# Optimization experiments

Hardware: AMD Instinct MI355X
Metric: run time of the kernel (lower is better)

Reference implementation:

```python
import jax, jax.numpy as jnp
import numpy as np

N = 100000      # num nodes
E = 1600000     # num edges
NFEAT = 512
NHID = 256
NCLASS = 32
K = 10
ALPHA = 0.1


def setup_inputs() -> dict:
    key = jax.random.key(0)
    ks = jax.random.split(key, 6)
    x = jax.random.normal(ks[0], (N, NFEAT), dtype=jnp.float32)
    edge_index = jax.random.randint(ks[1], (2, E), 0, N, dtype=jnp.int32)
    edge_attr = jax.random.uniform(ks[2], (E,), dtype=jnp.float32)
    # Linear params (Kaiming-ish scale)
    W_start = jax.random.normal(ks[3], (NFEAT, NHID), dtype=jnp.float32) * np.float32(1.0 / np.sqrt(NFEAT))
    b_start = jnp.zeros((NHID,), jnp.float32)
    W_end = jax.random.normal(ks[4], (NHID, NCLASS), dtype=jnp.float32) * np.float32(1.0 / np.sqrt(NHID))
    b_end = jnp.zeros((NCLASS,), jnp.float32)
    # GPR 'PPR' init coefficients: temp[k] = alpha*(1-alpha)^k, temp[K] = (1-alpha)^K
    temp = (ALPHA * (1.0 - ALPHA) ** np.arange(K + 1)).astype(np.float32)
    temp[-1] = np.float32((1.0 - ALPHA) ** K)
    temp = jnp.asarray(temp)
    return {"x": x, "edge_attr": edge_attr, "W_start": W_start, "b_start": b_start,
            "W_end": W_end, "b_end": b_end, "temp": temp, "edge_index": edge_index}


def gcn_norm(edge_index, edge_weight, num_nodes):
    # add self loops with weight 1 (PyG default fill_value=1)
    loop = jnp.arange(num_nodes, dtype=edge_index.dtype)
    ei = jnp.concatenate([edge_index, jnp.stack([loop, loop])], axis=1)   # [2, E+N]
    ew = jnp.concatenate([edge_weight, jnp.ones((num_nodes,), edge_weight.dtype)])
    row, col = ei[0], ei[1]
    deg = jax.ops.segment_sum(ew, col, num_segments=num_nodes)            # [N]
    dis = jnp.where(deg > 0, jax.lax.rsqrt(jnp.where(deg > 0, deg, 1.0)), 0.0)
    norm = dis[row] * ew * dis[col]                                       # [E+N]
    return ei, norm


def reference(x, edge_attr, W_start, b_start, W_end, b_end, temp, edge_index):
    # MLP front-end (eval mode: dropout is identity)
    h = jax.nn.relu(x @ W_start + b_start)        # [N, NHID]
    h = jax.nn.relu(h @ W_end + b_end)            # [N, NCLASS]
    ei, norm = gcn_norm(edge_index, edge_attr, N)
    row, col = ei[0], ei[1]
    hidden = h * temp[0]
    xk = h
    for k in range(K):
        # SpMM: gather messages norm * x[row], scatter-add at col
        xk = jax.ops.segment_sum(norm[:, None] * xk[row], col, num_segments=N)
        hidden = hidden + temp[k + 1] * xk
    return hidden
```

## Files before the change

kernel.cpp:

```cpp
#include <hip/hip_runtime.h>

typedef __attribute__((ext_vector_type(8))) short short8;
typedef __attribute__((ext_vector_type(4))) float f32x4;
typedef unsigned long long u64;

constexpr int NN = 100000;
constexpr int EE = 1600000;
constexpr int NF = 512;
constexpr int NH = 256;
constexpr int NC = 32;
constexpr int KP = 10;
constexpr int PKN = EE + 8 * NN;
constexpr int GB = 782;

__device__ __forceinline__ unsigned short f2bf(float f) {
  unsigned int u = __float_as_uint(f);
  u += 0x7FFFu + ((u >> 16) & 1u);
  return (unsigned short)(u >> 16);
}
__device__ __forceinline__ float bf2f(unsigned short s) {
  return __uint_as_float(((unsigned int)s) << 16);
}
__device__ __forceinline__ int padc(int c) { return (c + 7) & ~7; }

__device__ __forceinline__ short8 cvt8(float4 a0, float4 a1) {
  union { unsigned int u[4]; short8 s; } r;
  asm("v_cvt_pk_bf16_f32 %0, %1, %2" : "=v"(r.u[0]) : "v"(a0.x), "v"(a0.y));
  asm("v_cvt_pk_bf16_f32 %0, %1, %2" : "=v"(r.u[1]) : "v"(a0.z), "v"(a0.w));
  asm("v_cvt_pk_bf16_f32 %0, %1, %2" : "=v"(r.u[2]) : "v"(a1.x), "v"(a1.y));
  asm("v_cvt_pk_bf16_f32 %0, %1, %2" : "=v"(r.u[3]) : "v"(a1.z), "v"(a1.w));
  return r.s;
}

__device__ __forceinline__ void block_sync_lds() {
  asm volatile("s_waitcnt lgkmcnt(0)" ::: "memory");
  __builtin_amdgcn_s_barrier();
}

__global__ void prep_kernel(const float* __restrict__ Ws, const float* __restrict__ We,
                            unsigned short* __restrict__ Wt, unsigned short* __restrict__ Web,
                            u64* __restrict__ dc, u64* __restrict__ pk) {
  if (blockIdx.x < 32) {
    __shared__ float tile[64][65];
    const int k0 = (blockIdx.x >> 2) * 64;
    const int c0 = (blockIdx.x & 3) * 64;
    const int t = threadIdx.x;
    const int g = t >> 6, l = t & 63;
#pragma unroll
    for (int j = 0; j < 16; j++) {
      const int row = g * 16 + j;
      tile[row][l] = Ws[(size_t)(k0 + row) * NH + c0 + l];
    }
    __syncthreads();
    const int col = t >> 2, ks = (t & 3) * 16;
    union { unsigned short us[16]; short8 s8[2]; } st;
#pragma unroll
    for (int i = 0; i < 16; i++) st.us[i] = f2bf(tile[ks + i][col]);
    unsigned short* dst = Wt + (size_t)(c0 + col) * NF + k0 + ks;
    *reinterpret_cast<short8*>(dst) = st.s8[0];
    *reinterpret_cast<short8*>(dst + 8) = st.s8[1];
  } else if (blockIdx.x == 32) {
    const int t = threadIdx.x;
    const int col = t & 31, kb = (t >> 5) * 32;
#pragma unroll
    for (int i = 0; i < 32; i++)
      Web[(size_t)col * 256 + kb + i] = f2bf(We[(size_t)(kb + i) * NC + col]);
  } else {
    const int i = (blockIdx.x - 33) * 256 + threadIdx.x;
    if (i < NN) dc[i] = (1ULL << 44) | (1ULL << 32);
    for (int j = i; j < PKN; j += 391 * 256) pk[j] = 0;
  }
}

__global__ __launch_bounds__(512, 2) void gemm_deg_kernel(
    const float* __restrict__ X, const unsigned short* __restrict__ Wt,
    const float* __restrict__ bias, const unsigned short* __restrict__ Web,
    const float* __restrict__ be, const float* __restrict__ temp,
    unsigned short* __restrict__ x0b, float* __restrict__ out,
    const int* __restrict__ ei, const float* __restrict__ ew, u64* dc) {
  constexpr int PAD = 36;
  __shared__ __align__(16) unsigned short Asm[2][128 * PAD];
  __shared__ __align__(16) unsigned short Bsm[2][256 * PAD];
  const int tid = threadIdx.x;

  if (blockIdx.x >= GB) {
    const int e = (blockIdx.x - GB) * 512 + tid;
    if (e < EE) {
      const int col = ei[EE + e];
      u64 v = (1ULL << 44) | (u64)((double)ew[e] * 4294967296.0);
      atomicAdd(&dc[col], v);
    }
    return;
  }

  const int lane = tid & 63;
  const int w = tid >> 6;
  const int wm = w >> 2, wn = w & 3;
  const int l15 = lane & 15, kq = lane >> 4;
  const int m0 = blockIdx.x * 128;

  const int arl = tid >> 2, aq = tid & 3;
  int ar = m0 + arl; if (ar >= NN) ar = NN - 1;
  const float* aptr = X + (size_t)ar * NF + aq * 8;
  const int awr = arl * PAD + aq * 8;
  const int bcl = tid >> 1, bh = tid & 1;
  const unsigned short* bptr = Wt + (size_t)bcl * NF + bh * 16;
  const int bwr = bcl * PAD + bh * 16;

  f32x4 acc[4][4];
#pragma unroll
  for (int m = 0; m < 4; m++)
#pragma unroll
    for (int n = 0; n < 4; n++) acc[m][n] = (f32x4)0.0f;

  float4 ra[3][2]; short8 rb[3][2];

#define LOADR(ks, j) do { \
    ra[j][0] = *reinterpret_cast<const float4*>(aptr + (ks) * 32); \
    ra[j][1] = *reinterpret_cast<const float4*>(aptr + (ks) * 32 + 4); \
    rb[j][0] = *reinterpret_cast<const short8*>(bptr + (ks) * 32); \
    rb[j][1] = *reinterpret_cast<const short8*>(bptr + (ks) * 32 + 8); \
  } while (0)

#define STAGE(b, j) do { \
    *reinterpret_cast<short8*>(&Asm[b][awr]) = cvt8(ra[j][0], ra[j][1]); \
    *reinterpret_cast<short8*>(&Bsm[b][bwr]) = rb[j][0]; \
    *reinterpret_cast<short8*>(&Bsm[b][bwr + 8]) = rb[j][1]; \
  } while (0)

#define COMPUTE(b) do { \
    short8 af[4], bfr[4]; \
    _Pragma("unroll") \
    for (int mi = 0; mi < 4; mi++) \
      af[mi] = *reinterpret_cast<const short8*>(&Asm[b][(wm * 64 + mi * 16 + l15) * PAD + kq * 8]); \
    _Pragma("unroll") \
    for (int ni = 0; ni < 4; ni++) \
      bfr[ni] = *reinterpret_cast<const short8*>(&Bsm[b][(wn * 64 + ni * 16 + l15) * PAD + kq * 8]); \
    _Pragma("unroll") \
    for (int mi = 0; mi < 4; mi++) \
      _Pragma("unroll") \
      for (int ni = 0; ni < 4; ni++) \
        acc[mi][ni] = __builtin_amdgcn_mfma_f32_16x16x32_bf16(af[mi], bfr[ni], acc[mi][ni], 0, 0, 0); \
  } while (0)

  LOADR(0, 0);
  LOADR(1, 1);
  LOADR(2, 2);
  STAGE(0, 0);
  block_sync_lds();

#pragma unroll
  for (int p = 0; p < 16; p++) {
    if (p + 3 < 16) LOADR(p + 3, (p + 3) % 3);
    COMPUTE(p & 1);
    if (p + 1 < 16) STAGE((p + 1) & 1, (p + 1) % 3);
    block_sync_lds();
  }
#undef LOADR
#undef STAGE
#undef COMPUTE

  unsigned short* Ht = (unsigned short*)Bsm;
  f32x4 acc2[2];
  acc2[0] = (f32x4)0.0f; acc2[1] = (f32x4)0.0f;
  const unsigned short* wrow = Web + (size_t)l15 * 256 + kq * 8;
#pragma unroll
  for (int p2 = 0; p2 < 2; p2++) {
    block_sync_lds();
    if ((wn >> 1) == p2) {
#pragma unroll
      for (int ni = 0; ni < 4; ni++) {
        const int colg = wn * 64 + ni * 16 + l15;
        const float bsv = bias[colg];
        const int cl = colg - p2 * 128;
#pragma unroll
        for (int mi = 0; mi < 4; mi++)
#pragma unroll
          for (int i = 0; i < 4; i++) {
            const int row = wm * 64 + mi * 16 + kq * 4 + i;
            const float v = acc[mi][ni][i] + bsv;
            Ht[row * 136 + cl] = f2bf(v > 0.f ? v : 0.f);
          }
      }
    }
    block_sync_lds();
    const unsigned short* hr = Ht + (size_t)(w * 16 + l15) * 136 + kq * 8;
#pragma unroll
    for (int ks = 0; ks < 4; ks++) {
      short8 a  = *reinterpret_cast<const short8*>(hr + ks * 32);
      short8 b0 = *reinterpret_cast<const short8*>(wrow + p2 * 128 + ks * 32);
      short8 b1 = *reinterpret_cast<const short8*>(wrow + 16 * 256 + p2 * 128 + ks * 32);
      acc2[0] = __builtin_amdgcn_mfma_f32_16x16x32_bf16(a, b0, acc2[0], 0, 0, 0);
      acc2[1] = __builtin_amdgcn_mfma_f32_16x16x32_bf16(a, b1, acc2[1], 0, 0, 0);
    }
  }
  const float t0 = temp[0];
#pragma unroll
  for (int nt = 0; nt < 2; nt++) {
    const int col = nt * 16 + l15;
    const float bv = be[col];
#pragma unroll
    for (int i = 0; i < 4; i++) {
      const int row = m0 + w * 16 + kq * 4 + i;
      if (row < NN) {
        float v = acc2[nt][i] + bv;
        v = v > 0.f ? v : 0.f;
        x0b[(size_t)row * NC + col] = f2bf(v);
        out[(size_t)row * NC + col] = t0 * v;
      }
    }
  }
}

__global__ void dis_scan_kernel(const u64* __restrict__ dc, float* __restrict__ dis,
                                int* __restrict__ cnt, int* bsum) {
  __shared__ int ws[4];
  const int tid = threadIdx.x;
  int base = blockIdx.x * 1024 + tid * 4;
  int s = 0;
#pragma unroll
  for (int j = 0; j < 4; j++) {
    int i = base + j;
    if (i < NN) {
      u64 v = dc[i];
      int c = (int)(v >> 44);
      cnt[i] = c;
      float deg = (float)((double)(v & 0xFFFFFFFFFFFULL) * (1.0 / 4294967296.0));
      dis[i] = rsqrtf(deg);
      s += padc(c);
    }
  }
  for (int off = 32; off > 0; off >>= 1) s += __shfl_down(s, off);
  if ((tid & 63) == 0) ws[tid >> 6] = s;
  __syncthreads();
  if (tid == 0) bsum[blockIdx.x] = ws[0] + ws[1] + ws[2] + ws[3];
}

__global__ void scan3_kernel(const int* __restrict__ cnt, const int* __restrict__ bsum,
                             int* offs, int* cursor) {
  __shared__ int wsum[4];
  __shared__ int bofs_s;
  const int tid = threadIdx.x;
  const int lane = tid & 63, wv = tid >> 6;
  if (tid == 0) {
    int run = 0;
    for (int i = 0; i < (int)blockIdx.x; i++) run += bsum[i];
    bofs_s = run;
    if (blockIdx.x == 0) {
      int tot = 0;
      for (int i = 0; i < 98; i++) tot += bsum[i];
      offs[NN] = tot;
    }
  }
  int base = blockIdx.x * 1024 + tid * 4;
  int v[4]; int s = 0;
#pragma unroll
  for (int j = 0; j < 4; j++) { int i = base + j; v[j] = (i < NN) ? padc(cnt[i]) : 0; s += v[j]; }
  int incl = s;
  for (int off = 1; off < 64; off <<= 1) {
    int t = __shfl_up(incl, off);
    if (lane >= off) incl += t;
  }
  if (lane == 63) wsum[wv] = incl;
  __syncthreads();
  int woff = bofs_s;
  for (int w = 0; w < wv; w++) woff += wsum[w];
  int excl = woff + incl - s;
#pragma unroll
  for (int j = 0; j < 4; j++) {
    int i = base + j;
    if (i < NN) { offs[i] = excl; cursor[i] = excl; }
    excl += v[j];
  }
}

__global__ void fill_kernel(const int* __restrict__ ei, const float* __restrict__ ew,
                            const float* __restrict__ dis, int* cursor,
                            u64* __restrict__ pk) {
  int t = blockIdx.x * 256 + threadIdx.x;
  if (t < EE) {
    int r = ei[t], c = ei[EE + t];
    int slot = atomicAdd(&cursor[c], 1);
    unsigned int wb = __float_as_uint(dis[r] * ew[t] * dis[c]);
    pk[slot] = (u64)(unsigned int)r | ((u64)wb << 32);
  } else if (t < EE + NN) {
    int i = t - EE;
    int slot = atomicAdd(&cursor[i], 1);
    float d = dis[i];
    unsigned int wb = __float_as_uint(d * d);
    pk[slot] = (u64)(unsigned int)i | ((u64)wb << 32);
  }
}

__global__ __launch_bounds__(256) void spmm_kernel(
    const int* __restrict__ offs, const u64* __restrict__ pk,
    const unsigned short* __restrict__ xin, unsigned short* __restrict__ xout) {
  const int tid = threadIdx.x;
  const int node = blockIdx.x * 32 + (tid >> 3);
  const int fq = (tid & 7) * 4;
  const int s = offs[node], e = offs[node + 1];
  float a0 = 0.f, a1 = 0.f, a2 = 0.f, a3 = 0.f;
  for (int j = s; j < e; j += 8) {
    ulonglong2 p01 = *reinterpret_cast<const ulonglong2*>(pk + j);
    ulonglong2 p23 = *reinterpret_cast<const ulonglong2*>(pk + j + 2);
    ulonglong2 p45 = *reinterpret_cast<const ulonglong2*>(pk + j + 4);
    ulonglong2 p67 = *reinterpret_cast<const ulonglong2*>(pk + j + 6);
    const u64 p[8] = {p01.x, p01.y, p23.x, p23.y, p45.x, p45.y, p67.x, p67.y};
    u64 q[8];
#pragma unroll
    for (int i = 0; i < 8; i++)
      q[i] = *reinterpret_cast<const u64*>(xin + (size_t)(unsigned int)p[i] * NC + fq);
#pragma unroll
    for (int i = 0; i < 8; i++) {
      const float w = __uint_as_float((unsigned int)(p[i] >> 32));
      a0 += w * bf2f((unsigned short)(q[i]));
      a1 += w * bf2f((unsigned short)(q[i] >> 16));
      a2 += w * bf2f((unsigned short)(q[i] >> 32));
      a3 += w * bf2f((unsigned short)(q[i] >> 48));
    }
  }
  unsigned int lo, hi;
  asm("v_cvt_pk_bf16_f32 %0, %1, %2" : "=v"(lo) : "v"(a0), "v"(a1));
  asm("v_cvt_pk_bf16_f32 %0, %1, %2" : "=v"(hi) : "v"(a2), "v"(a3));
  *reinterpret_cast<u64*>(xout + (size_t)node * NC + fq) =
      (u64)lo | ((u64)hi << 32);
}

__global__ __launch_bounds__(256) void spmm_wsum_kernel(
    const int* __restrict__ offs, const u64* __restrict__ pk,
    const unsigned short* __restrict__ xin,
    const unsigned short* __restrict__ SL,
    float* __restrict__ out, const float* __restrict__ temp) {
  const int tid = threadIdx.x;
  const int node = blockIdx.x * 32 + (tid >> 3);
  const int fq = (tid & 7) * 4;
  const int s = offs[node], e = offs[node + 1];
  float a0 = 0.f, a1 = 0.f, a2 = 0.f, a3 = 0.f;
  for (int j = s; j < e; j += 8) {
    ulonglong2 p01 = *reinterpret_cast<const ulonglong2*>(pk + j);
    ulonglong2 p23 = *reinterpret_cast<const ulonglong2*>(pk + j + 2);
    ulonglong2 p45 = *reinterpret_cast<const ulonglong2*>(pk + j + 4);
    ulonglong2 p67 = *reinterpret_cast<const ulonglong2*>(pk + j + 6);
    const u64 p[8] = {p01.x, p01.y, p23.x, p23.y, p45.x, p45.y, p67.x, p67.y};
    u64 q[8];
#pragma unroll
    for (int i = 0; i < 8; i++)
      q[i] = *reinterpret_cast<const u64*>(xin + (size_t)(unsigned int)p[i] * NC + fq);
#pragma unroll
    for (int i = 0; i < 8; i++) {
      const float w = __uint_as_float((unsigned int)(p[i] >> 32));
      a0 += w * bf2f((unsigned short)(q[i]));
      a1 += w * bf2f((unsigned short)(q[i] >> 16));
      a2 += w * bf2f((unsigned short)(q[i] >> 32));
      a3 += w * bf2f((unsigned short)(q[i] >> 48));
    }
  }
  const size_t ob = (size_t)node * NC + fq;
  float4 o = *reinterpret_cast<const float4*>(out + ob);
  const float t10 = temp[10];
  float r0 = o.x + t10 * a0, r1 = o.y + t10 * a1;
  float r2 = o.z + t10 * a2, r3 = o.w + t10 * a3;
#pragma unroll
  for (int k = 0; k < 8; k++) {
    const float tk = temp[k + 1];
    u64 q = *reinterpret_cast<const u64*>(SL + (size_t)k * NN * NC + ob);
    r0 += tk * bf2f((unsigned short)(q));
    r1 += tk * bf2f((unsigned short)(q >> 16));
    r2 += tk * bf2f((unsigned short)(q >> 32));
    r3 += tk * bf2f((unsigned short)(q >> 48));
  }
  {
    const float tk = temp[9];
    u64 q = *reinterpret_cast<const u64*>(xin + ob);
    r0 += tk * bf2f((unsigned short)(q));
    r1 += tk * bf2f((unsigned short)(q >> 16));
    r2 += tk * bf2f((unsigned short)(q >> 32));
    r3 += tk * bf2f((unsigned short)(q >> 48));
  }
  *reinterpret_cast<float4*>(out + ob) = make_float4(r0, r1, r2, r3);
}

extern "C" void kernel_launch(void* const* d_in, const int* in_sizes, int n_in,
                              void* d_out, int out_size, void* d_ws, size_t ws_size,
                              hipStream_t stream) {
  const float* X    = (const float*)d_in[0];
  const float* EA   = (const float*)d_in[1];
  const float* Ws   = (const float*)d_in[2];
  const float* bs   = (const float*)d_in[3];
  const float* We   = (const float*)d_in[4];
  const float* be   = (const float*)d_in[5];
  const float* temp = (const float*)d_in[6];
  const int*   ei   = (const int*)d_in[7];
  float* out = (float*)d_out;

  size_t off = 0;
  auto alloc = [&](size_t n) { void* p = (char*)d_ws + off; off += (n + 255) & ~(size_t)255; return p; };
  unsigned short* Wt  = (unsigned short*)alloc((size_t)NF * NH * 2);
  unsigned short* Web = (unsigned short*)alloc((size_t)NH * NC * 2);
  unsigned short* SL  = (unsigned short*)alloc((size_t)NN * NH * 2);
  unsigned short* x0b = (unsigned short*)alloc((size_t)NN * NC * 2);
  unsigned short* xk8 = (unsigned short*)alloc((size_t)NN * NC * 2);
  u64*   dc   = (u64*)alloc((size_t)NN * 8);
  float* dis  = (float*)alloc((size_t)NN * 4);
  int*   cnt  = (int*)alloc((size_t)NN * 4);
  int*   offs = (int*)alloc((size_t)(NN + 1) * 4);
  int*   cursor = (int*)alloc((size_t)NN * 4);
  int*   bsum = (int*)alloc(98 * 4);
  u64*   pk   = (u64*)alloc((size_t)PKN * 8);

  prep_kernel<<<424, 256, 0, stream>>>(Ws, We, Wt, Web, dc, pk);

  gemm_deg_kernel<<<GB + 3125, 512, 0, stream>>>(X, Wt, bs, Web, be, temp,
                                                 x0b, out, ei, EA, dc);

  dis_scan_kernel<<<98, 256, 0, stream>>>(dc, dis, cnt, bsum);
  scan3_kernel<<<98, 256, 0, stream>>>(cnt, bsum, offs, cursor);
  fill_kernel<<<6641, 256, 0, stream>>>(ei, EA, dis, cursor, pk);

  auto slice = [&](int k) -> unsigned short* {
    return (k < 8) ? SL + (size_t)k * NN * NC : xk8;
  };
  const unsigned short* xin = x0b;
  for (int k = 0; k < KP - 1; k++) {
    spmm_kernel<<<3125, 256, 0, stream>>>(offs, pk, xin, slice(k));
    xin = slice(k);
  }
  spmm_wsum_kernel<<<3125, 256, 0, stream>>>(offs, pk, xk8, SL, out, temp);
}
```

Baseline: 475.5 us.

## Co-schedule CSR fill with GEMM and move degree atomics into prep

The degree-accumulation atomics move out of the GEMM launch and into the prep kernel, with the degree counter zeroed by a memset. The self-loop contribution is now added in the scan instead of being pre-seeded. The CSR fill, which was a separate kernel after the scan, now runs as extra blocks inside the GEMM launch, so the atomic-heavy fill overlaps the dense matmul. This removes one launch and aims to hide the fill's latency behind GEMM work, at the cost of a larger prep kernel and a memset that sit on the critical path before the scan.

```diff
diff --git a/kernel.cpp b/kernel.cpp
--- a/kernel.cpp
+++ b/kernel.cpp
@@ -12,6 +12,7 @@
 constexpr int KP = 10;
 constexpr int PKN = EE + 8 * NN;
 constexpr int GB = 782;
+constexpr int FB = 3321;
 
 __device__ __forceinline__ unsigned short f2bf(float f) {
   unsigned int u = __float_as_uint(f);
@@ -39,6 +40,7 @@
 
 __global__ void prep_kernel(const float* __restrict__ Ws, const float* __restrict__ We,
                             unsigned short* __restrict__ Wt, unsigned short* __restrict__ Web,
+                            const int* __restrict__ ei, const float* __restrict__ ew,
                             u64* __restrict__ dc, u64* __restrict__ pk) {
   if (blockIdx.x < 32) {
     __shared__ float tile[64][65];
@@ -66,29 +68,41 @@
     for (int i = 0; i < 32; i++)
       Web[(size_t)col * 256 + kb + i] = f2bf(We[(size_t)(kb + i) * NC + col]);
   } else {
-    const int i = (blockIdx.x - 33) * 256 + threadIdx.x;
-    if (i < NN) dc[i] = (1ULL << 44) | (1ULL << 32);
-    for (int j = i; j < PKN; j += 391 * 256) pk[j] = 0;
-  }
-}
-
-__global__ __launch_bounds__(512, 2) void gemm_deg_kernel(
+    const int gid = (blockIdx.x - 33) * 256 + threadIdx.x;
+    if (gid < EE) {
+      const int col = ei[EE + gid];
+      u64 v = (1ULL << 44) | (u64)((double)ew[gid] * 4294967296.0);
+      atomicAdd(&dc[col], v);
+    }
+    for (int j = gid; j < PKN; j += 6250 * 256) pk[j] = 0;
+  }
+}
+
+__global__ __launch_bounds__(512, 2) void gemm_fill_kernel(
     const float* __restrict__ X, const unsigned short* __restrict__ Wt,
     const float* __restrict__ bias, const unsigned short* __restrict__ Web,
     const float* __restrict__ be, const float* __restrict__ temp,
     unsigned short* __restrict__ x0b, float* __restrict__ out,
-    const int* __restrict__ ei, const float* __restrict__ ew, u64* dc) {
+    const int* __restrict__ ei, const float* __restrict__ ew,
+    const float* __restrict__ dis, int* cursor, u64* __restrict__ pk) {
   constexpr int PAD = 36;
   __shared__ __align__(16) unsigned short Asm[2][128 * PAD];
   __shared__ __align__(16) unsigned short Bsm[2][256 * PAD];
   const int tid = threadIdx.x;
 
   if (blockIdx.x >= GB) {
-    const int e = (blockIdx.x - GB) * 512 + tid;
-    if (e < EE) {
-      const int col = ei[EE + e];
-      u64 v = (1ULL << 44) | (u64)((double)ew[e] * 4294967296.0);
-      atomicAdd(&dc[col], v);
+    const int t = (blockIdx.x - GB) * 512 + tid;
+    if (t < EE) {
+      int r = ei[t], c = ei[EE + t];
+      int slot = atomicAdd(&cursor[c], 1);
+      unsigned int wb = __float_as_uint(dis[r] * ew[t] * dis[c]);
+      pk[slot] = (u64)(unsigned int)r | ((u64)wb << 32);
+    } else if (t < EE + NN) {
+      int i = t - EE;
+      int slot = atomicAdd(&cursor[i], 1);
+      float d = dis[i];
+      unsigned int wb = __float_as_uint(d * d);
+      pk[slot] = (u64)(unsigned int)i | ((u64)wb << 32);
     }
     return;
   }
@@ -223,9 +237,9 @@
     int i = base + j;
     if (i < NN) {
       u64 v = dc[i];
-      int c = (int)(v >> 44);
+      int c = (int)(v >> 44) + 1;
       cnt[i] = c;
-      float deg = (float)((double)(v & 0xFFFFFFFFFFFULL) * (1.0 / 4294967296.0));
+      float deg = (float)((double)(v & 0xFFFFFFFFFFFULL) * (1.0 / 4294967296.0) + 1.0);
       dis[i] = rsqrtf(deg);
       s += padc(c);
     }
@@ -271,24 +285,6 @@
     int i = base + j;
     if (i < NN) { offs[i] = excl; cursor[i] = excl; }
     excl += v[j];
-  }
-}
-
-__global__ void fill_kernel(const int* __restrict__ ei, const float* __restrict__ ew,
-                            const float* __restrict__ dis, int* cursor,
-                            u64* __restrict__ pk) {
-  int t = blockIdx.x * 256 + threadIdx.x;
-  if (t < EE) {
-    int r = ei[t], c = ei[EE + t];
-    int slot = atomicAdd(&cursor[c], 1);
-    unsigned int wb = __float_as_uint(dis[r] * ew[t] * dis[c]);
-    pk[slot] = (u64)(unsigned int)r | ((u64)wb << 32);
-  } else if (t < EE + NN) {
-    int i = t - EE;
-    int slot = atomicAdd(&cursor[i], 1);
-    float d = dis[i];
-    unsigned int wb = __float_as_uint(d * d);
-    pk[slot] = (u64)(unsigned int)i | ((u64)wb << 32);
   }
 }
 
@@ -408,14 +404,15 @@
   int*   bsum = (int*)alloc(98 * 4);
   u64*   pk   = (u64*)alloc((size_t)PKN * 8);
 
-  prep_kernel<<<424, 256, 0, stream>>>(Ws, We, Wt, Web, dc, pk);
-
-  gemm_deg_kernel<<<GB + 3125, 512, 0, stream>>>(X, Wt, bs, Web, be, temp,
-                                                 x0b, out, ei, EA, dc);
+  hipMemsetAsync(dc, 0, (size_t)NN * 8, stream);
+
+  prep_kernel<<<6283, 256, 0, stream>>>(Ws, We, Wt, Web, ei, EA, dc, pk);
 
   dis_scan_kernel<<<98, 256, 0, stream>>>(dc, dis, cnt, bsum);
   scan3_kernel<<<98, 256, 0, stream>>>(cnt, bsum, offs, cursor);
-  fill_kernel<<<6641, 256, 0, stream>>>(ei, EA, dis, cursor, pk);
+
+  gemm_fill_kernel<<<GB + FB, 512, 0, stream>>>(X, Wt, bs, Web, be, temp,
+                                                x0b, out, ei, EA, dis, cursor, pk);
 
   auto slice = [&](int k) -> unsigned short* {
     return (k < 8) ? SL + (size_t)k * NN * NC : xk8;
```

New measurement: 480.0 us. No clear change (+0.9%).
